# Performance work log

Hardware: AMD Instinct MI355X
Metric: run time of the kernel (lower is better)

Reference implementation:

```python
import jax, jax.numpy as jnp
import numpy as np

NPOINT, RADIUS, NSAMPLE, EPS = 1024, 0.2, 32, 1e-5


def furthest_point_sample(xyz, npoint):
    # xyz: [B,N,3] -> idx [B,npoint] int32. Sequential FPS starting at index 0
    # (matches pointnet2 CUDA kernel initialization).
    B, N, _ = xyz.shape
    dist0 = jnp.full((B, N), 1e10, xyz.dtype)
    far0 = jnp.zeros((B,), jnp.int32)
    idx0 = jnp.zeros((B, npoint), jnp.int32)  # idx[:,0] = 0

    def body(i, state):
        idx, dist, far = state
        centroid = jnp.take_along_axis(xyz, far[:, None, None], axis=1)  # [B,1,3]
        d = jnp.sum((xyz - centroid) ** 2, axis=-1)                       # [B,N]
        dist = jnp.minimum(dist, d)
        far = jnp.argmax(dist, axis=1).astype(jnp.int32)
        return idx.at[:, i].set(far), dist, far

    idx, _, _ = jax.lax.fori_loop(1, npoint, body, (idx0, dist0, far0))
    return idx


def ball_query(radius, nsample, xyz, new_xyz):
    # xyz [B,N,3], new_xyz [B,S,3] -> idx [B,S,nsample] int32.
    # First nsample points (in original order) within radius; slots with no
    # neighbor are filled with the first found index (standard pointnet2 semantics).
    B, N, _ = xyz.shape
    S = new_xyz.shape[1]
    d2 = (jnp.sum(new_xyz ** 2, -1)[:, :, None]
          + jnp.sum(xyz ** 2, -1)[:, None, :]
          - 2.0 * jnp.einsum('bsc,bnc->bsn', new_xyz, xyz))  # [B,S,N]
    grp = jnp.broadcast_to(jnp.arange(N, dtype=jnp.int32), (B, S, N))
    grp = jnp.where(d2 > radius * radius, N, grp)
    grp = jnp.sort(grp, axis=-1)[:, :, :nsample]
    first = grp[:, :, :1]
    return jnp.where(grp == N, first, grp)


def _gather(pts, idx):
    # pts [B,N,C], idx [B,...] -> [B,...,C]
    return jax.vmap(lambda p, i: p[i])(pts, idx)


def setup_inputs() -> dict:
    key = jax.random.key(0)
    ks = jax.random.split(key, 32)
    B, N, D = 16, 4096, 64
    mlp = [64, 64, 128]
    inp = {
        'xyz': jax.random.uniform(ks[0], (B, N, 3), jnp.float32),
        'points': jax.random.normal(ks[1], (B, N, D), jnp.float32),
    }
    cprev = 3 + D
    for i, cout in enumerate(mlp):
        kk = ks[2 + 4 * i: 6 + 4 * i]
        inp[f'W{i}'] = jax.random.normal(kk[0], (cout, cprev), jnp.float32) / np.float32(np.sqrt(cprev))
        inp[f'b{i}'] = jax.random.normal(kk[1], (cout,), jnp.float32) * 0.01
        inp[f'g{i}'] = 1.0 + 0.1 * jax.random.normal(kk[2], (cout,), jnp.float32)
        inp[f'beta{i}'] = 0.1 * jax.random.normal(kk[3], (cout,), jnp.float32)
        inp[f'm{i}'] = jnp.zeros((cout,), jnp.float32)
        inp[f'v{i}'] = jnp.ones((cout,), jnp.float32)
        cprev = cout
    return inp


def reference(xyz, points, W0, b0, g0, beta0, m0, v0,
              W1, b1, g1, beta1, m1, v1,
              W2, b2, g2, beta2, m2, v2):
    fps_idx = furthest_point_sample(xyz, NPOINT)
    new_xyz = _gather(xyz, fps_idx)                       # [B,S,3]
    idx = ball_query(RADIUS, NSAMPLE, xyz, new_xyz)       # [B,S,K]
    grouped_xyz = _gather(xyz, idx)                       # [B,S,K,3]
    grouped_norm = grouped_xyz - new_xyz[:, :, None, :]
    grouped_pts = _gather(points, idx)                    # [B,S,K,D]
    h = jnp.concatenate([grouped_norm, grouped_pts], axis=-1)  # [B,S,K,3+D]
    layers = [(W0, b0, g0, beta0, m0, v0), (W1, b1, g1, beta1, m1, v1), (W2, b2, g2, beta2, m2, v2)]
    for W, b, g, be, m, v in layers:
        h = jnp.einsum('oc,bskc->bsko', W, h) + b          # 1x1 conv
        h = (h - m) * (g * jax.lax.rsqrt(v + EPS)) + be    # eval-mode BN
        h = jax.nn.relu(h)
    new_points = jnp.max(h, axis=2)                        # max over nsample -> [B,S,Cout]
    return new_xyz, new_points
```

## Files before the change

### kernel.cpp

```cpp
#include <hip/hip_runtime.h>

#define N_PTS  4096
#define N_CENT 1024
#define K_S    32
#define EPSV   1e-5f

typedef __attribute__((ext_vector_type(8))) short short8;
typedef __attribute__((ext_vector_type(4))) float floatx4;
typedef __attribute__((ext_vector_type(2))) float float2v;

__device__ inline unsigned short bf1(float x) {
  unsigned u = __float_as_uint(x);
  u += 0x7fffu + ((u >> 16) & 1u);
  return (unsigned short)(u >> 16);
}
__device__ inline unsigned pkbf(float a, float b) {
  return (unsigned)bf1(a) | ((unsigned)bf1(b) << 16);
}

__global__ void prep_kernel(const float* __restrict__ W0, const float* __restrict__ b0,
                            const float* __restrict__ g0, const float* __restrict__ be0,
                            const float* __restrict__ m0, const float* __restrict__ v0,
                            const float* __restrict__ W1, const float* __restrict__ b1,
                            const float* __restrict__ g1, const float* __restrict__ be1,
                            const float* __restrict__ m1, const float* __restrict__ v1,
                            const float* __restrict__ W2, const float* __restrict__ b2,
                            const float* __restrict__ g2, const float* __restrict__ be2,
                            const float* __restrict__ m2, const float* __restrict__ v2,
                            unsigned char* __restrict__ wsb) {
  const int stride = gridDim.x * blockDim.x;
  const int tid = blockIdx.x * blockDim.x + threadIdx.x;
  unsigned short* WB0 = (unsigned short*)wsb;
  unsigned short* WB1 = (unsigned short*)(wsb + 12288);
  unsigned short* WB2 = (unsigned short*)(wsb + 20480);
  float* Bf0 = (float*)(wsb + 36864);
  float* Bf1 = (float*)(wsb + 37120);
  float* Bf2 = (float*)(wsb + 37376);
  for (int i = tid; i < 64 * 96; i += stride) {
    int o = i / 96, k = i - o * 96;
    float s = g0[o] * rsqrtf(v0[o] + EPSV);
    float val = 0.0f;
    if (k < 64) val = W0[o * 67 + 3 + k] * s;
    else if (k < 67) val = W0[o * 67 + (k - 64)] * s;
    WB0[i] = bf1(val);
  }
  for (int i = tid; i < 64; i += stride) {
    float s = g0[i] * rsqrtf(v0[i] + EPSV);
    Bf0[i] = (b0[i] - m0[i]) * s + be0[i];
  }
  for (int i = tid; i < 64 * 64; i += stride) {
    int o = i >> 6;
    float s = g1[o] * rsqrtf(v1[o] + EPSV);
    WB1[i] = bf1(W1[i] * s);
  }
  for (int i = tid; i < 64; i += stride) {
    float s = g1[i] * rsqrtf(v1[i] + EPSV);
    Bf1[i] = (b1[i] - m1[i]) * s + be1[i];
  }
  for (int i = tid; i < 128 * 64; i += stride) {
    int o = i >> 6;
    float s = g2[o] * rsqrtf(v2[o] + EPSV);
    WB2[i] = bf1(W2[i] * s);
  }
  for (int i = tid; i < 128; i += stride) {
    float s = g2[i] * rsqrtf(v2[i] + EPSV);
    Bf2[i] = (b2[i] - m2[i]) * s + be2[i];
  }
}

#define DPP_STEP(CTRL)                                                               \
  {                                                                                  \
    unsigned lo2 = (unsigned)__builtin_amdgcn_update_dpp(                            \
        0, (int)(unsigned)key, (CTRL), 0xf, 0xf, false);                             \
    unsigned hi2 = (unsigned)__builtin_amdgcn_update_dpp(                            \
        0, (int)(unsigned)(key >> 32), (CTRL), 0xf, 0xf, false);                     \
    unsigned long long nk = ((unsigned long long)hi2 << 32) | lo2;                   \
    if (nk > key) key = nk;                                                          \
  }

__launch_bounds__(256)
__global__ void fps_kernel(const float* __restrict__ xyz, float* __restrict__ new_xyz) {
#pragma clang fp contract(off)
  const int b = blockIdx.x;
  const int tid = threadIdx.x;
  const int lane = tid & 63, wv = tid >> 6;
  const float* X = xyz + (size_t)b * N_PTS * 3;
  float* outc = new_xyz + (size_t)b * N_CENT * 3;
  __shared__ float lx[N_PTS], ly[N_PTS], lz[N_PTS];
  __shared__ unsigned long long rkey[2][4];
  float2v px[8], py[8], pz[8], dist[8];
#pragma unroll
  for (int j = 0; j < 16; ++j) {
    int p = j * 256 + tid;
    float x = X[p * 3 + 0], y = X[p * 3 + 1], z = X[p * 3 + 2];
    lx[p] = x; ly[p] = y; lz[p] = z;
    int t = j >> 1;
    if ((j & 1) == 0) { px[t].x = x; py[t].x = y; pz[t].x = z; dist[t].x = 1e10f; }
    else              { px[t].y = x; py[t].y = y; pz[t].y = z; dist[t].y = 1e10f; }
  }
  __syncthreads();
  int far = 0;
  for (int i = 1; i < N_CENT; ++i) {
    float cx = lx[far], cy = ly[far], cz = lz[far];
    if (lane == 0) {
      float* o = outc + (i - 1) * 3;
      o[0] = cx; o[1] = cy; o[2] = cz;
    }
    float2v cx2 = {cx, cx}, cy2 = {cy, cy}, cz2 = {cz, cz};
#pragma unroll
    for (int t = 0; t < 8; ++t) {
      float2v dx = px[t] - cx2, dy = py[t] - cy2, dz = pz[t] - cz2;
      float2v d2 = dx * dx + dy * dy + dz * dz;
      dist[t].x = fminf(dist[t].x, d2.x);
      dist[t].y = fminf(dist[t].y, d2.y);
    }
    float v[8];
    int jj[8];
#pragma unroll
    for (int t = 0; t < 8; ++t) {
      bool r = dist[t].y > dist[t].x;
      v[t] = r ? dist[t].y : dist[t].x;
      jj[t] = r ? (2 * t + 1) : (2 * t);
    }
#pragma unroll
    for (int s = 1; s < 8; s <<= 1)
#pragma unroll
      for (int t = 0; t < 8; t += 2 * s) {
        if (v[t + s] > v[t]) { v[t] = v[t + s]; jj[t] = jj[t + s]; }
      }
    const int bi = (jj[0] << 8) + tid;
    unsigned long long key =
        ((unsigned long long)__float_as_uint(v[0]) << 32) | (unsigned)(~bi);
    DPP_STEP(0x111);
    DPP_STEP(0x112);
    DPP_STEP(0x114);
    DPP_STEP(0x118);
    DPP_STEP(0x142);
    DPP_STEP(0x143);
    const int par = i & 1;
    if (lane == 63) rkey[par][wv] = key;
    __syncthreads();
    unsigned long long k0 = rkey[par][0], k1 = rkey[par][1];
    unsigned long long k2 = rkey[par][2], k3 = rkey[par][3];
    if (k1 > k0) k0 = k1;
    if (k3 > k2) k2 = k3;
    if (k2 > k0) k0 = k2;
    far = (int)~(unsigned)k0;
  }
  if (lane == 0) {
    float* o = outc + (N_CENT - 1) * 3;
    o[0] = lx[far]; o[1] = ly[far]; o[2] = lz[far];
  }
}

__launch_bounds__(256)
__global__ void query_kernel(const float* __restrict__ xyz,
                             const float* __restrict__ new_xyz,
                             int* __restrict__ nid_g) {
#pragma clang fp contract(off)
  const int blk = blockIdx.x;
  const int b = blk >> 7;
  const int s0 = (blk & 127) << 3;
  const int tid = threadIdx.x;
  const int wv = tid >> 6, lane = tid & 63;
  const float* Xb = xyz + (size_t)b * N_PTS * 3;
  const float r2 = (float)(0.2 * 0.2);
  const int sA = s0 + wv * 2, sB = sA + 1;
  float cxA = new_xyz[((size_t)b * N_CENT + sA) * 3 + 0];
  float cyA = new_xyz[((size_t)b * N_CENT + sA) * 3 + 1];
  float czA = new_xyz[((size_t)b * N_CENT + sA) * 3 + 2];
  float cxB = new_xyz[((size_t)b * N_CENT + sB) * 3 + 0];
  float cyB = new_xyz[((size_t)b * N_CENT + sB) * 3 + 1];
  float czB = new_xyz[((size_t)b * N_CENT + sB) * 3 + 2];
  float scA = cxA * cxA + cyA * cyA + czA * czA;
  float scB = cxB * cxB + cyB * cyB + czB * czB;
  int* outA = nid_g + ((size_t)b * N_CENT + sA) * K_S;
  int* outB = nid_g + ((size_t)b * N_CENT + sB) * K_S;
  int cntA = 0, cntB = 0, firstA = 0, firstB = 0;
  for (int base = 0; base < N_PTS && (cntA < K_S || cntB < K_S); base += 64) {
    int p = base + lane;
    float x = Xb[p * 3 + 0], y = Xb[p * 3 + 1], z = Xb[p * 3 + 2];
    float sp = x * x + y * y + z * z;
    float dtA = __builtin_fmaf(czA, z, __builtin_fmaf(cyA, y, cxA * x));
    float dtB = __builtin_fmaf(czB, z, __builtin_fmaf(cyB, y, cxB * x));
    float d2A = (scA + sp) - 2.0f * dtA;
    float d2B = (scB + sp) - 2.0f * dtB;
    bool inA = !(d2A > r2);
    bool inB = !(d2B > r2);
    unsigned long long mA = __ballot(inA);
    unsigned long long mB = __ballot(inB);
    if (cntA == 0 && mA != 0ull) firstA = base + __builtin_ctzll(mA);
    if (cntB == 0 && mB != 0ull) firstB = base + __builtin_ctzll(mB);
    unsigned long long below = (1ull << lane) - 1ull;
    int posA = cntA + __popcll(mA & below);
    int posB = cntB + __popcll(mB & below);
    if (inA && posA < K_S) outA[posA] = p;
    if (inB && posB < K_S) outB[posB] = p;
    cntA += __popcll(mA);
    cntB += __popcll(mB);
  }
  if (cntA < K_S)
    for (int j = cntA + lane; j < K_S; j += 64) outA[j] = firstA;
  if (cntB < K_S)
    for (int j = cntB + lane; j < K_S; j += 64) outB[j] = firstB;
}

__launch_bounds__(256)
__global__ void mlp_kernel(const float* __restrict__ xyz,
                           const float* __restrict__ points,
                           const float* __restrict__ new_xyz,
                           const unsigned char* __restrict__ wsb,
                           const int* __restrict__ nid_g,
                           float* __restrict__ out_pts) {
  __shared__ __align__(16) unsigned short h[256 * 104];
  const int blk = blockIdx.x;
  const int b = blk >> 7;
  const int s0 = (blk & 127) << 3;
  const int tid = threadIdx.x;
  const float* Xb = xyz + (size_t)b * N_PTS * 3;

  {
    const int s = s0 + (tid >> 5);
    const int id = nid_g[((size_t)b * N_CENT + s0) * K_S + tid];
    float cx = new_xyz[((size_t)b * N_CENT + s) * 3 + 0];
    float cy = new_xyz[((size_t)b * N_CENT + s) * 3 + 1];
    float cz = new_xyz[((size_t)b * N_CENT + s) * 3 + 2];
    float gx = Xb[id * 3 + 0] - cx;
    float gy = Xb[id * 3 + 1] - cy;
    float gz = Xb[id * 3 + 2] - cz;
    unsigned short* hrow = &h[tid * 104];
    const float4* P = (const float4*)(points + ((size_t)b * N_PTS + id) * 64);
#pragma unroll
    for (int c8 = 0; c8 < 8; ++c8) {
      float4 u = P[2 * c8], v = P[2 * c8 + 1];
      uint4 w4;
      w4.x = pkbf(u.x, u.y); w4.y = pkbf(u.z, u.w);
      w4.z = pkbf(v.x, v.y); w4.w = pkbf(v.z, v.w);
      *(uint4*)(hrow + c8 * 8) = w4;
    }
    uint4 t4;
    t4.x = pkbf(gx, gy); t4.y = pkbf(gz, 0.0f); t4.z = 0u; t4.w = 0u;
    *(uint4*)(hrow + 64) = t4;
    uint4 z4; z4.x = z4.y = z4.z = z4.w = 0u;
    *(uint4*)(hrow + 72) = z4;
    *(uint4*)(hrow + 80) = z4;
    *(uint4*)(hrow + 88) = z4;
  }
  __syncthreads();

  const int lane = tid & 63, w = tid >> 6;
  const int col = lane & 15, kq = lane >> 4;
  const unsigned short* WB0 = (const unsigned short*)wsb;
  const unsigned short* WB1 = (const unsigned short*)(wsb + 12288);
  const unsigned short* WB2 = (const unsigned short*)(wsb + 20480);
  const float* Bf0 = (const float*)(wsb + 36864);
  const float* Bf1 = (const float*)(wsb + 37120);
  const float* Bf2 = (const float*)(wsb + 37376);

  {
    const int o = w * 16 + col;
    float bias = Bf0[o];
    floatx4 acc[16];
#pragma unroll
    for (int mt = 0; mt < 16; ++mt) acc[mt] = floatx4{bias, bias, bias, bias};
#pragma unroll
    for (int c = 0; c < 3; ++c) {
      short8 bf = *(const short8*)(WB0 + o * 96 + kq * 8 + 32 * c);
#pragma unroll
      for (int mt = 0; mt < 16; ++mt) {
        short8 af = *(const short8*)(&h[(mt * 16 + col) * 104 + kq * 8 + 32 * c]);
        acc[mt] = __builtin_amdgcn_mfma_f32_16x16x32_bf16(af, bf, acc[mt], 0, 0, 0);
      }
    }
    __syncthreads();
#pragma unroll
    for (int mt = 0; mt < 16; ++mt)
#pragma unroll
      for (int r = 0; r < 4; ++r)
        h[(mt * 16 + kq * 4 + r) * 104 + o] = bf1(fmaxf(acc[mt][r], 0.0f));
    __syncthreads();
  }

  {
    const int o = w * 16 + col;
    float bias = Bf1[o];
    floatx4 acc[16];
#pragma unroll
    for (int mt = 0; mt < 16; ++mt) acc[mt] = floatx4{bias, bias, bias, bias};
#pragma unroll
    for (int c = 0; c < 2; ++c) {
      short8 bf = *(const short8*)(WB1 + o * 64 + kq * 8 + 32 * c);
#pragma unroll
      for (int mt = 0; mt < 16; ++mt) {
        short8 af = *(const short8*)(&h[(mt * 16 + col) * 104 + kq * 8 + 32 * c]);
        acc[mt] = __builtin_amdgcn_mfma_f32_16x16x32_bf16(af, bf, acc[mt], 0, 0, 0);
      }
    }
    __syncthreads();
#pragma unroll
    for (int mt = 0; mt < 16; ++mt)
#pragma unroll
      for (int r = 0; r < 4; ++r)
        h[(mt * 16 + kq * 4 + r) * 104 + o] = bf1(fmaxf(acc[mt][r], 0.0f));
    __syncthreads();
  }

  {
    const int oA = w * 32 + col;
    const int oB = oA + 16;
    float biasA = Bf2[oA], biasB = Bf2[oB];
    floatx4 accA[16], accB[16];
#pragma unroll
    for (int mt = 0; mt < 16; ++mt) {
      accA[mt] = floatx4{biasA, biasA, biasA, biasA};
      accB[mt] = floatx4{biasB, biasB, biasB, biasB};
    }
#pragma unroll
    for (int c = 0; c < 2; ++c) {
      short8 bfA = *(const short8*)(WB2 + oA * 64 + kq * 8 + 32 * c);
      short8 bfB = *(const short8*)(WB2 + oB * 64 + kq * 8 + 32 * c);
#pragma unroll
      for (int mt = 0; mt < 16; ++mt) {
        short8 af = *(const short8*)(&h[(mt * 16 + col) * 104 + kq * 8 + 32 * c]);
        accA[mt] = __builtin_amdgcn_mfma_f32_16x16x32_bf16(af, bfA, accA[mt], 0, 0, 0);
        accB[mt] = __builtin_amdgcn_mfma_f32_16x16x32_bf16(af, bfB, accB[mt], 0, 0, 0);
      }
    }
#pragma unroll
    for (int mtp = 0; mtp < 8; ++mtp) {
      float vA = fmaxf(fmaxf(fmaxf(accA[2 * mtp][0], accA[2 * mtp + 1][0]),
                             fmaxf(accA[2 * mtp][1], accA[2 * mtp + 1][1])),
                       fmaxf(fmaxf(accA[2 * mtp][2], accA[2 * mtp + 1][2]),
                             fmaxf(accA[2 * mtp][3], accA[2 * mtp + 1][3])));
      float vB = fmaxf(fmaxf(fmaxf(accB[2 * mtp][0], accB[2 * mtp + 1][0]),
                             fmaxf(accB[2 * mtp][1], accB[2 * mtp + 1][1])),
                       fmaxf(fmaxf(accB[2 * mtp][2], accB[2 * mtp + 1][2]),
                             fmaxf(accB[2 * mtp][3], accB[2 * mtp + 1][3])));
      vA = fmaxf(vA, __shfl_xor(vA, 16)); vA = fmaxf(vA, __shfl_xor(vA, 32));
      vB = fmaxf(vB, __shfl_xor(vB, 16)); vB = fmaxf(vB, __shfl_xor(vB, 32));
      vA = fmaxf(vA, 0.0f); vB = fmaxf(vB, 0.0f);
      if (lane < 16) {
        float* op = out_pts + ((size_t)(b * N_CENT + s0 + mtp)) * 128;
        op[oA] = vA;
        op[oB] = vB;
      }
    }
  }
}

extern "C" void kernel_launch(void* const* d_in, const int* in_sizes, int n_in,
                              void* d_out, int out_size, void* d_ws, size_t ws_size,
                              hipStream_t stream) {
  const float* xyz = (const float*)d_in[0];
  const float* points = (const float*)d_in[1];
  float* out = (float*)d_out;
  float* new_xyz = out;
  float* out_pts = out + 16 * 1024 * 3;
  unsigned char* wsb = (unsigned char*)d_ws;
  int* nid_g = (int*)(wsb + 65536);

  prep_kernel<<<64, 256, 0, stream>>>(
      (const float*)d_in[2], (const float*)d_in[3], (const float*)d_in[4],
      (const float*)d_in[5], (const float*)d_in[6], (const float*)d_in[7],
      (const float*)d_in[8], (const float*)d_in[9], (const float*)d_in[10],
      (const float*)d_in[11], (const float*)d_in[12], (const float*)d_in[13],
      (const float*)d_in[14], (const float*)d_in[15], (const float*)d_in[16],
      (const float*)d_in[17], (const float*)d_in[18], (const float*)d_in[19], wsb);
  fps_kernel<<<16, 256, 0, stream>>>(xyz, new_xyz);
  query_kernel<<<2048, 256, 0, stream>>>(xyz, new_xyz, nid_g);
  mlp_kernel<<<2048, 256, 0, stream>>>(xyz, points, new_xyz, wsb, nid_g, out_pts);
}
```

Baseline: 807.6 us.

## Widen FPS blocks to 1024 threads with DPP cross-wave reduction

The furthest-point-sampling kernel now runs 1024 threads per batch instead of 256. Each thread holds 4 points instead of 16, which shortens the serial per-iteration distance update and argmax. The 16 per-wave keys are combined with a DPP row reduction and a readlane, replacing the scalar compare chain. The trade-off is more waves taking part in each of the 1023 barriers, and the per-iteration latency may still be dominated by the barrier and LDS traffic.

```diff
diff --git a/kernel.cpp b/kernel.cpp
--- a/kernel.cpp
+++ b/kernel.cpp
@@ -68,17 +68,17 @@
   }
 }
 
-#define DPP_STEP(CTRL)                                                               \
+#define DPP_MAXK(VAR, CTRL)                                                          \
   {                                                                                  \
     unsigned lo2 = (unsigned)__builtin_amdgcn_update_dpp(                            \
-        0, (int)(unsigned)key, (CTRL), 0xf, 0xf, false);                             \
+        0, (int)(unsigned)(VAR), (CTRL), 0xf, 0xf, false);                           \
     unsigned hi2 = (unsigned)__builtin_amdgcn_update_dpp(                            \
-        0, (int)(unsigned)(key >> 32), (CTRL), 0xf, 0xf, false);                     \
+        0, (int)(unsigned)((VAR) >> 32), (CTRL), 0xf, 0xf, false);                   \
     unsigned long long nk = ((unsigned long long)hi2 << 32) | lo2;                   \
-    if (nk > key) key = nk;                                                          \
-  }
-
-__launch_bounds__(256)
+    if (nk > (VAR)) (VAR) = nk;                                                      \
+  }
+
+__launch_bounds__(1024)
 __global__ void fps_kernel(const float* __restrict__ xyz, float* __restrict__ new_xyz) {
 #pragma clang fp contract(off)
   const int b = blockIdx.x;
@@ -87,11 +87,11 @@
   const float* X = xyz + (size_t)b * N_PTS * 3;
   float* outc = new_xyz + (size_t)b * N_CENT * 3;
   __shared__ float lx[N_PTS], ly[N_PTS], lz[N_PTS];
-  __shared__ unsigned long long rkey[2][4];
-  float2v px[8], py[8], pz[8], dist[8];
-#pragma unroll
-  for (int j = 0; j < 16; ++j) {
-    int p = j * 256 + tid;
+  __shared__ unsigned long long rkey[2][16];
+  float2v px[2], py[2], pz[2], dist[2];
+#pragma unroll
+  for (int j = 0; j < 4; ++j) {
+    int p = j * 1024 + tid;
     float x = X[p * 3 + 0], y = X[p * 3 + 1], z = X[p * 3 + 2];
     lx[p] = x; ly[p] = y; lz[p] = z;
     int t = j >> 1;
@@ -108,44 +108,39 @@
     }
     float2v cx2 = {cx, cx}, cy2 = {cy, cy}, cz2 = {cz, cz};
 #pragma unroll
-    for (int t = 0; t < 8; ++t) {
+    for (int t = 0; t < 2; ++t) {
       float2v dx = px[t] - cx2, dy = py[t] - cy2, dz = pz[t] - cz2;
       float2v d2 = dx * dx + dy * dy + dz * dz;
       dist[t].x = fminf(dist[t].x, d2.x);
       dist[t].y = fminf(dist[t].y, d2.y);
     }
-    float v[8];
-    int jj[8];
-#pragma unroll
-    for (int t = 0; t < 8; ++t) {
-      bool r = dist[t].y > dist[t].x;
-      v[t] = r ? dist[t].y : dist[t].x;
-      jj[t] = r ? (2 * t + 1) : (2 * t);
-    }
-#pragma unroll
-    for (int s = 1; s < 8; s <<= 1)
-#pragma unroll
-      for (int t = 0; t < 8; t += 2 * s) {
-        if (v[t + s] > v[t]) { v[t] = v[t + s]; jj[t] = jj[t + s]; }
-      }
-    const int bi = (jj[0] << 8) + tid;
+    bool r0 = dist[0].y > dist[0].x;
+    float v0 = r0 ? dist[0].y : dist[0].x;
+    int j0 = r0 ? 1 : 0;
+    bool r1 = dist[1].y > dist[1].x;
+    float v1 = r1 ? dist[1].y : dist[1].x;
+    int j1 = r1 ? 3 : 2;
+    bool r2 = v1 > v0;
+    float vb = r2 ? v1 : v0;
+    int jb = r2 ? j1 : j0;
+    const int bi = (jb << 10) + tid;
     unsigned long long key =
-        ((unsigned long long)__float_as_uint(v[0]) << 32) | (unsigned)(~bi);
-    DPP_STEP(0x111);
-    DPP_STEP(0x112);
-    DPP_STEP(0x114);
-    DPP_STEP(0x118);
-    DPP_STEP(0x142);
-    DPP_STEP(0x143);
+        ((unsigned long long)__float_as_uint(vb) << 32) | (unsigned)(~bi);
+    DPP_MAXK(key, 0x111);
+    DPP_MAXK(key, 0x112);
+    DPP_MAXK(key, 0x114);
+    DPP_MAXK(key, 0x118);
+    DPP_MAXK(key, 0x142);
+    DPP_MAXK(key, 0x143);
     const int par = i & 1;
     if (lane == 63) rkey[par][wv] = key;
     __syncthreads();
-    unsigned long long k0 = rkey[par][0], k1 = rkey[par][1];
-    unsigned long long k2 = rkey[par][2], k3 = rkey[par][3];
-    if (k1 > k0) k0 = k1;
-    if (k3 > k2) k2 = k3;
-    if (k2 > k0) k0 = k2;
-    far = (int)~(unsigned)k0;
+    unsigned long long k = rkey[par][lane & 15];
+    DPP_MAXK(k, 0x111);
+    DPP_MAXK(k, 0x112);
+    DPP_MAXK(k, 0x114);
+    DPP_MAXK(k, 0x118);
+    far = (int)~(unsigned)__builtin_amdgcn_readlane((int)(unsigned)k, 15);
   }
   if (lane == 0) {
     float* o = outc + (N_CENT - 1) * 3;
@@ -366,7 +361,7 @@
       (const float*)d_in[11], (const float*)d_in[12], (const float*)d_in[13],
       (const float*)d_in[14], (const float*)d_in[15], (const float*)d_in[16],
       (const float*)d_in[17], (const float*)d_in[18], (const float*)d_in[19], wsb);
-  fps_kernel<<<16, 256, 0, stream>>>(xyz, new_xyz);
+  fps_kernel<<<16, 1024, 0, stream>>>(xyz, new_xyz);
   query_kernel<<<2048, 256, 0, stream>>>(xyz, new_xyz, nid_g);
   mlp_kernel<<<2048, 256, 0, stream>>>(xyz, points, new_xyz, wsb, nid_g, out_pts);
 }
```

After: 1.036 ms. +28.3%, slower.

## Carry winner coordinates through FPS reduction instead of shared-memory point lookup

Applied to the files above, without the earlier changes.

The FPS loop now tracks the coordinates of each thread's farthest candidate alongside its key. The winning lane in each wave publishes its key and xyz to a small shared slot, and the four wave results are reduced with DPP and readlane. This removes the dependent shared-memory lookup of the new centroid from the per-iteration critical path and drops the full point copy in LDS. Centroids are buffered in LDS and written to global memory once at the end, instead of with a scalar store each iteration. It adds extra selects per thread to carry coordinates through the reduction.

```diff
diff --git a/kernel.cpp b/kernel.cpp
--- a/kernel.cpp
+++ b/kernel.cpp
@@ -68,15 +68,24 @@
   }
 }
 
-#define DPP_STEP(CTRL)                                                               \
+#define DPP_MAXK(VAR, CTRL)                                                          \
   {                                                                                  \
     unsigned lo2 = (unsigned)__builtin_amdgcn_update_dpp(                            \
-        0, (int)(unsigned)key, (CTRL), 0xf, 0xf, false);                             \
+        0, (int)(unsigned)(VAR), (CTRL), 0xf, 0xf, false);                           \
     unsigned hi2 = (unsigned)__builtin_amdgcn_update_dpp(                            \
-        0, (int)(unsigned)(key >> 32), (CTRL), 0xf, 0xf, false);                     \
+        0, (int)(unsigned)((VAR) >> 32), (CTRL), 0xf, 0xf, false);                   \
     unsigned long long nk = ((unsigned long long)hi2 << 32) | lo2;                   \
-    if (nk > key) key = nk;                                                          \
-  }
+    if (nk > (VAR)) (VAR) = nk;                                                      \
+  }
+
+__device__ inline unsigned long long rl64(unsigned long long v, int l) {
+  unsigned lo = (unsigned)__builtin_amdgcn_readlane((int)(unsigned)v, l);
+  unsigned hi = (unsigned)__builtin_amdgcn_readlane((int)(unsigned)(v >> 32), l);
+  return ((unsigned long long)hi << 32) | lo;
+}
+__device__ inline float rlf(float v, int l) {
+  return __int_as_float(__builtin_amdgcn_readlane(__float_as_int(v), l));
+}
 
 __launch_bounds__(256)
 __global__ void fps_kernel(const float* __restrict__ xyz, float* __restrict__ new_xyz) {
@@ -86,26 +95,21 @@
   const int lane = tid & 63, wv = tid >> 6;
   const float* X = xyz + (size_t)b * N_PTS * 3;
   float* outc = new_xyz + (size_t)b * N_CENT * 3;
-  __shared__ float lx[N_PTS], ly[N_PTS], lz[N_PTS];
-  __shared__ unsigned long long rkey[2][4];
+  __shared__ float cent[N_CENT * 3];
+  __shared__ unsigned long long kslot[2][4];
+  __shared__ float4 xslot[2][4];
   float2v px[8], py[8], pz[8], dist[8];
 #pragma unroll
   for (int j = 0; j < 16; ++j) {
     int p = j * 256 + tid;
     float x = X[p * 3 + 0], y = X[p * 3 + 1], z = X[p * 3 + 2];
-    lx[p] = x; ly[p] = y; lz[p] = z;
     int t = j >> 1;
     if ((j & 1) == 0) { px[t].x = x; py[t].x = y; pz[t].x = z; dist[t].x = 1e10f; }
     else              { px[t].y = x; py[t].y = y; pz[t].y = z; dist[t].y = 1e10f; }
   }
-  __syncthreads();
-  int far = 0;
+  float cx = X[0], cy = X[1], cz = X[2];
+  if (tid == 0) { cent[0] = cx; cent[1] = cy; cent[2] = cz; }
   for (int i = 1; i < N_CENT; ++i) {
-    float cx = lx[far], cy = ly[far], cz = lz[far];
-    if (lane == 0) {
-      float* o = outc + (i - 1) * 3;
-      o[0] = cx; o[1] = cy; o[2] = cz;
-    }
     float2v cx2 = {cx, cx}, cy2 = {cy, cy}, cz2 = {cz, cz};
 #pragma unroll
     for (int t = 0; t < 8; ++t) {
@@ -114,43 +118,58 @@
       dist[t].x = fminf(dist[t].x, d2.x);
       dist[t].y = fminf(dist[t].y, d2.y);
     }
-    float v[8];
+    float v[8], xw[8], yw[8], zw[8];
     int jj[8];
 #pragma unroll
     for (int t = 0; t < 8; ++t) {
       bool r = dist[t].y > dist[t].x;
       v[t] = r ? dist[t].y : dist[t].x;
       jj[t] = r ? (2 * t + 1) : (2 * t);
+      xw[t] = r ? px[t].y : px[t].x;
+      yw[t] = r ? py[t].y : py[t].x;
+      zw[t] = r ? pz[t].y : pz[t].x;
     }
 #pragma unroll
     for (int s = 1; s < 8; s <<= 1)
 #pragma unroll
       for (int t = 0; t < 8; t += 2 * s) {
-        if (v[t + s] > v[t]) { v[t] = v[t + s]; jj[t] = jj[t + s]; }
+        if (v[t + s] > v[t]) {
+          v[t] = v[t + s]; jj[t] = jj[t + s];
+          xw[t] = xw[t + s]; yw[t] = yw[t + s]; zw[t] = zw[t + s];
+        }
       }
     const int bi = (jj[0] << 8) + tid;
-    unsigned long long key =
+    const unsigned long long mykey =
         ((unsigned long long)__float_as_uint(v[0]) << 32) | (unsigned)(~bi);
-    DPP_STEP(0x111);
-    DPP_STEP(0x112);
-    DPP_STEP(0x114);
-    DPP_STEP(0x118);
-    DPP_STEP(0x142);
-    DPP_STEP(0x143);
+    unsigned long long key = mykey;
+    DPP_MAXK(key, 0x111);
+    DPP_MAXK(key, 0x112);
+    DPP_MAXK(key, 0x114);
+    DPP_MAXK(key, 0x118);
+    DPP_MAXK(key, 0x142);
+    DPP_MAXK(key, 0x143);
     const int par = i & 1;
-    if (lane == 63) rkey[par][wv] = key;
-    __syncthreads();
-    unsigned long long k0 = rkey[par][0], k1 = rkey[par][1];
-    unsigned long long k2 = rkey[par][2], k3 = rkey[par][3];
-    if (k1 > k0) k0 = k1;
-    if (k3 > k2) k2 = k3;
-    if (k2 > k0) k0 = k2;
-    far = (int)~(unsigned)k0;
-  }
-  if (lane == 0) {
-    float* o = outc + (N_CENT - 1) * 3;
-    o[0] = lx[far]; o[1] = ly[far]; o[2] = lz[far];
-  }
+    const unsigned long long kwave = rl64(key, 63);
+    if (mykey == kwave) {
+      kslot[par][wv] = mykey;
+      xslot[par][wv] = make_float4(xw[0], yw[0], zw[0], 0.0f);
+    }
+    __syncthreads();
+    unsigned long long ks = kslot[par][lane & 3];
+    float4 c4 = xslot[par][lane & 3];
+    unsigned long long kk = ks;
+    DPP_MAXK(kk, 0x111);
+    DPP_MAXK(kk, 0x112);
+    const unsigned long long kmax = rl64(kk, 3);
+    const unsigned long long mwin = __ballot(ks == kmax);
+    const int sw = (int)__builtin_ctzll(mwin);
+    cx = rlf(c4.x, sw); cy = rlf(c4.y, sw); cz = rlf(c4.z, sw);
+    if (tid == 0) {
+      cent[i * 3 + 0] = cx; cent[i * 3 + 1] = cy; cent[i * 3 + 2] = cz;
+    }
+  }
+  __syncthreads();
+  for (int t = tid; t < N_CENT * 3; t += 256) outc[t] = cent[t];
 }
 
 __launch_bounds__(256)
```

Result: slower. 1.354 ms (median of 2 runs) (+67.6%).
